# Kernel tuning notes

Hardware: AMD Instinct MI355X
Metric: run time of the kernel (lower is better)

Reference implementation:

```python
import jax, jax.numpy as jnp
import numpy as np

INPUT_DIM = 1024
NUM_HEADS = 16
HEAD_DIM = INPUT_DIM // NUM_HEADS


def setup_inputs() -> dict:
    key = jax.random.key(0)
    ks = jax.random.split(key, 9)
    d = INPUT_DIM
    s = 1.0 / np.sqrt(d)
    x = jax.random.normal(ks[0], (2, 2048, d), dtype=jnp.float32)
    # nn.Linear default init ~ U(-1/sqrt(in), 1/sqrt(in)); weights stored as (out, in), we keep (in, out)
    Wq = jax.random.uniform(ks[1], (d, d), jnp.float32, -s, s)
    bq = jax.random.uniform(ks[2], (d,), jnp.float32, -s, s)
    Wk = jax.random.uniform(ks[3], (d, d), jnp.float32, -s, s)
    bk = jax.random.uniform(ks[4], (d,), jnp.float32, -s, s)
    Wv = jax.random.uniform(ks[5], (d, d), jnp.float32, -s, s)
    bv = jax.random.uniform(ks[6], (d,), jnp.float32, -s, s)
    Wo = jax.random.uniform(ks[7], (d, d), jnp.float32, -s, s)
    bo = jax.random.uniform(ks[8], (d,), jnp.float32, -s, s)
    return {"x": x, "Wq": Wq, "bq": bq, "Wk": Wk, "bk": bk, "Wv": Wv, "bv": bv, "Wo": Wo, "bo": bo}


def reference(x, Wq, bq, Wk, bk, Wv, bv, Wo, bo):
    b, t, d = x.shape
    h, hd = NUM_HEADS, HEAD_DIM
    # projections -> [b, h, t, hd]
    q = (x @ Wq + bq).reshape(b, t, h, hd).transpose(0, 2, 1, 3)
    k = (x @ Wk + bk).reshape(b, t, h, hd).transpose(0, 2, 1, 3)
    v = (x @ Wv + bv).reshape(b, t, h, hd).transpose(0, 2, 1, 3)
    scores = jnp.einsum('bhqd,bhkd->bhqk', q, k) / jnp.sqrt(jnp.float32(hd))
    probs = jax.nn.softmax(scores, axis=-1)
    out = jnp.einsum('bhqk,bhkd->bhqd', probs, v)
    out = out.transpose(0, 2, 1, 3).reshape(b, t, d)
    return out @ Wo + bo
```

## Files before the change

kernel.cpp:

```cpp
#include <hip/hip_runtime.h>
#include <math.h>


#define BATCH 2
#define SEQ   2048
#define DIM   1024
#define NHEAD 16
#define HDIM  64
#define MROWS (BATCH * SEQ)
#define BH    (BATCH * NHEAD)
#define NKT   (SEQ / 64)

typedef __attribute__((ext_vector_type(4))) float     floatx4;
typedef __attribute__((ext_vector_type(4))) float     float4v;
typedef __attribute__((ext_vector_type(8))) _Float16  half8;
typedef __attribute__((ext_vector_type(4))) _Float16  half4;
typedef __attribute__((ext_vector_type(2))) __fp16    fp16x2;
typedef __attribute__((ext_vector_type(4))) unsigned  uint4v;

#define SOFT_C 5.77078016f
#define QSCALE 0.18033688f

#if __has_builtin(__builtin_amdgcn_exp2f)
#define EXP2F(x) __builtin_amdgcn_exp2f(x)
#else
#define EXP2F(x) exp2f(x)
#endif

__device__ __forceinline__ void gload16(const void* g, void* l) {
    __builtin_amdgcn_global_load_lds(
        (const __attribute__((address_space(1))) unsigned int*)g,
        (__attribute__((address_space(3))) unsigned int*)l, 16, 0, 0);
}

__device__ __forceinline__ unsigned pk2(float a, float b) {
    fp16x2 v = __builtin_amdgcn_cvt_pkrtz(a, b);
    return __builtin_bit_cast(unsigned, v);
}

__device__ __forceinline__ void plswap(unsigned &a, unsigned &b) {
#if __has_builtin(__builtin_amdgcn_permlane32_swap) && __has_builtin(__builtin_amdgcn_permlane16_swap)
    auto r32 = __builtin_amdgcn_permlane32_swap(a, b, false, false);
    auto r16 = __builtin_amdgcn_permlane16_swap(r32[0], r32[1], false, false);
    a = r16[0]; b = r16[1];
#else
    asm volatile("s_nop 1\n\t"
                 "v_permlane32_swap_b32 %0, %1\n\t"
                 "s_nop 1\n\t"
                 "v_permlane16_swap_b32 %0, %1\n\t"
                 "s_nop 1"
                 : "+v"(a), "+v"(b));
#endif
}

__global__ __launch_bounds__(256) void prep(
    const float* __restrict__ x,
    const float* __restrict__ Wq, const float* __restrict__ Wk,
    const float* __restrict__ Wv, const float* __restrict__ Wo,
    _Float16* __restrict__ xh,
    _Float16* __restrict__ Wqt, _Float16* __restrict__ Wkt,
    _Float16* __restrict__ Wvt, _Float16* __restrict__ Wot)
{
    const int tid = threadIdx.x;
    if (blockIdx.z == 4) {
        const int bid = blockIdx.y * 16 + blockIdx.x;
        #pragma unroll
        for (int it = 0; it < 8; ++it) {
            const size_t i = (((size_t)it * 256 + bid) * 256 + tid) * 8;
            float4v a = *(const float4v*)(x + i);
            float4v b = *(const float4v*)(x + i + 4);
            half8 o;
            #pragma unroll
            for (int c = 0; c < 4; ++c) { o[c] = (_Float16)a[c]; o[4+c] = (_Float16)b[c]; }
            *(half8*)(xh + i) = o;
        }
        return;
    }
    __shared__ float tile[64][65];
    const float* W; _Float16* o;
    switch (blockIdx.z) {
        case 0: W = Wq; o = Wqt; break;
        case 1: W = Wk; o = Wkt; break;
        case 2: W = Wv; o = Wvt; break;
        default: W = Wo; o = Wot; break;
    }
    const int n0 = blockIdx.x * 64, k0 = blockIdx.y * 64;
    #pragma unroll
    for (int p = 0; p < 16; ++p) {
        int idx = tid + p * 256;
        int r = idx >> 6, c = idx & 63;
        tile[r][c] = W[(size_t)(k0 + r) * DIM + n0 + c];
    }
    __syncthreads();
    #pragma unroll
    for (int p = 0; p < 16; ++p) {
        int idx = tid + p * 256;
        int r = idx >> 6, c = idx & 63;
        o[(size_t)(n0 + r) * DIM + k0 + c] = (_Float16)tile[c][r];
    }
}

__device__ __forceinline__ void gemm_core16(
    const _Float16* __restrict__ Ap, const _Float16* __restrict__ Bp,
    int m0, int n0, _Float16* AL, _Float16* BL, floatx4 acc[4][4])
{
    const int tid  = threadIdx.x;
    const int wave = tid >> 6;
    const int lane = tid & 63;
    const int li   = lane & 15;
    const int quad = lane >> 4;
    const int wm   = (wave >> 1) * 64;
    const int wn   = (wave & 1) * 64;

    for (int kt = 0; kt < DIM / 64; ++kt) {
        __syncthreads();
        const int k0 = kt * 64;
        #pragma unroll
        for (int p = 0; p < 4; ++p) {
            int s = tid + p * 256;
            int r = s >> 3, ks = s & 7;
            int kg = (ks ^ (r & 7)) << 3;
            int ldsb = (wave * 64 + p * 256) * 8;
            gload16(Ap + (size_t)(m0 + r) * DIM + k0 + kg, AL + ldsb);
            gload16(Bp + (size_t)(n0 + r) * DIM + k0 + kg, BL + ldsb);
        }
        __syncthreads();

        half8 a[4][2], b[4][2];
        #pragma unroll
        for (int i = 0; i < 4; ++i) {
            int ra = (wm + i * 16 + li) << 6;
            int rb = (wn + i * 16 + li) << 6;
            #pragma unroll
            for (int h = 0; h < 2; ++h) {
                a[i][h] = *(const half8*)(AL + ra + (((h * 4 + quad) ^ (li & 7)) << 3));
                b[i][h] = *(const half8*)(BL + rb + (((h * 4 + quad) ^ (li & 7)) << 3));
            }
        }
        #pragma unroll
        for (int i = 0; i < 4; ++i)
            #pragma unroll
            for (int j = 0; j < 4; ++j) {
                acc[i][j] = __builtin_amdgcn_mfma_f32_16x16x32_f16(a[i][0], b[j][0], acc[i][j], 0, 0, 0);
                acc[i][j] = __builtin_amdgcn_mfma_f32_16x16x32_f16(a[i][1], b[j][1], acc[i][j], 0, 0, 0);
            }
    }
}

__global__ __launch_bounds__(256, 2) void qkv_mfma(
    const _Float16* __restrict__ xh,
    const _Float16* __restrict__ Wqt, const _Float16* __restrict__ Wkt,
    const _Float16* __restrict__ Wvt,
    const float* __restrict__ bq, const float* __restrict__ bk,
    const float* __restrict__ bv,
    _Float16* __restrict__ Qh, _Float16* __restrict__ Kh,
    _Float16* __restrict__ Vth)
{
    __shared__ __align__(16) _Float16 SH[128 * 128];
    _Float16* AL = SH;
    _Float16* BL = SH + 128 * 64;

    const int bid = blockIdx.x + 8 * (blockIdx.y + 32 * blockIdx.z);
    const int swz = (bid & 7) * 96 + (bid >> 3);
    const int bx  = swz & 7;
    const int by  = (swz >> 3) & 31;
    const int z   = swz >> 8;

    const _Float16* Bp; const float* bias;
    if (z == 0)      { Bp = Wqt; bias = bq; }
    else if (z == 1) { Bp = Wkt; bias = bk; }
    else             { Bp = Wvt; bias = bv; }

    const int m0 = by * 128, n0 = bx * 128;

    floatx4 acc[4][4];
    #pragma unroll
    for (int i = 0; i < 4; ++i)
        #pragma unroll
        for (int j = 0; j < 4; ++j) acc[i][j] = (floatx4){0.f, 0.f, 0.f, 0.f};

    gemm_core16(xh, Bp, m0, n0, AL, BL, acc);

    const int tid = threadIdx.x, wave = tid >> 6, lane = tid & 63;
    const int li = lane & 15, quad = lane >> 4;
    const int wm = (wave >> 1) * 64, wn = (wave & 1) * 64;
    const int bb = m0 >> 11, t0 = m0 & 2047;

    if (z != 2) {
        _Float16* out = (z == 0) ? Qh : Kh;
        const float sc = (z == 0) ? QSCALE : 1.0f;
        #pragma unroll
        for (int i = 0; i < 4; ++i)
            #pragma unroll
            for (int j = 0; j < 4; ++j) {
                int n = n0 + wn + j * 16 + li;
                int h = n >> 6, hd = n & 63;
                float b_ = bias[n];
                #pragma unroll
                for (int r = 0; r < 4; ++r) {
                    int m = m0 + wm + i * 16 + quad * 4 + r;
                    int t = m & 2047;
                    out[(((size_t)(bb * NHEAD + h) * SEQ) + t) * HDIM + hd] =
                        (_Float16)((acc[i][j][r] + b_) * sc);
                }
            }
    } else {
        __syncthreads();
        #pragma unroll
        for (int i = 0; i < 4; ++i)
            #pragma unroll
            for (int j = 0; j < 4; ++j) {
                int n = wn + j * 16 + li;
                float b_ = bias[n0 + n];
                half4 w;
                #pragma unroll
                for (int r = 0; r < 4; ++r) w[r] = (_Float16)(acc[i][j][r] + b_);
                int col  = wm + i * 16 + quad * 4;
                int colp = ((((col >> 3) ^ (n & 7)) << 3)) | (col & 7);
                *(half4*)(SH + n * 128 + colp) = w;
            }
        __syncthreads();
        #pragma unroll
        for (int p = 0; p < 8; ++p) {
            int idx = p * 256 + tid;
            int v = idx >> 4, c8 = (idx & 15) * 8;
            int c8p = (((c8 >> 3) ^ (v & 7)) << 3);
            half8 w = *(const half8*)(SH + v * 128 + c8p);
            int n = n0 + v;
            int h = n >> 6, hd = n & 63;
            *(half8*)(Vth + ((size_t)(bb * NHEAD + h) * HDIM + hd) * SEQ + t0 + c8) = w;
        }
    }
}

__global__ __launch_bounds__(256, 2) void attn(
    const _Float16* __restrict__ Q, const _Float16* __restrict__ K,
    const _Float16* __restrict__ Vt,
    _Float16* __restrict__ Ctx)
{
    __shared__ __align__(16) _Float16 Ks[2][64 * 64];
    __shared__ __align__(16) _Float16 Vs[2][64 * 64];

    const int tid  = threadIdx.x;
    const int wave = tid >> 6;
    const int lane = tid & 63;
    const int li   = lane & 15;
    const int quad = lane >> 4;

    const int bid = blockIdx.x + 16 * blockIdx.y;
    const int swz = (bid & 7) * 64 + (bid >> 3);
    const int q0  = (swz & 15) * 128;
    const int bh  = swz >> 4;
    const int b   = bh >> 4, h = bh & 15;

    half8 qa[2][2];
    #pragma unroll
    for (int nq = 0; nq < 2; ++nq) {
        size_t qrow = ((size_t)bh * SEQ + q0 + wave * 32 + nq * 16 + li) * HDIM;
        qa[nq][0] = *(const half8*)(Q + qrow + quad * 8);
        qa[nq][1] = *(const half8*)(Q + qrow + 32 + quad * 8);
    }

    half8 onesA;
    {
        _Float16 v = (li == 0) ? (_Float16)1.0f : (_Float16)0.0f;
        #pragma unroll
        for (int c = 0; c < 8; ++c) onesA[c] = v;
    }

    floatx4 O[4][2];
    floatx4 rsacc[2];
    #pragma unroll
    for (int nq = 0; nq < 2; ++nq) {
        rsacc[nq] = (floatx4){0.f, 0.f, 0.f, 0.f};
        #pragma unroll
        for (int i = 0; i < 4; ++i) O[i][nq] = (floatx4){0.f, 0.f, 0.f, 0.f};
    }

    const _Float16* Kbh = K  + (size_t)bh * SEQ * HDIM;
    const _Float16* Vbh = Vt + (size_t)bh * HDIM * SEQ;

    auto stage = [&](int buf, int kt_) {
        const _Float16* Kg = Kbh + (size_t)kt_ * 64 * HDIM;
        const _Float16* Vg = Vbh + kt_ * 64;
        _Float16* Kl = &Ks[buf][0];
        _Float16* Vl = &Vs[buf][0];
        #pragma unroll
        for (int p = 0; p < 2; ++p) {
            int s = tid + p * 256;
            int r = s >> 3, ks = s & 7;
            int kg = (ks ^ (r & 7)) << 3;
            int ldsb = (wave * 64 + p * 256) * 8;
            gload16(Kg + r * HDIM + kg, Kl + ldsb);
            gload16(Vg + (size_t)r * SEQ + kg, Vl + ldsb);
        }
    };

    auto qk_phase = [&](const _Float16* Kc, const _Float16* Vc,
                        half8 (&pbN)[2][2], half8 (&vfN)[4][2]) {
        unsigned R[2][4][2];
        #pragma unroll
        for (int mb = 0; mb < 4; ++mb) {
            int row = (mb * 16 + li) << 6;
            half8 a0 = *(const half8*)(Kc + row + ((quad ^ (li & 7)) << 3));
            half8 a1 = *(const half8*)(Kc + row + (((quad + 4) ^ (li & 7)) << 3));
            #pragma unroll
            for (int nq = 0; nq < 2; ++nq) {
                floatx4 st = (floatx4){-SOFT_C, -SOFT_C, -SOFT_C, -SOFT_C};
                st = __builtin_amdgcn_mfma_f32_16x16x32_f16(a0, qa[nq][0], st, 0, 0, 0);
                st = __builtin_amdgcn_mfma_f32_16x16x32_f16(a1, qa[nq][1], st, 0, 0, 0);
                R[nq][mb][0] = pk2(EXP2F(st[0]), EXP2F(st[1]));
                R[nq][mb][1] = pk2(EXP2F(st[2]), EXP2F(st[3]));
            }
        }
        #pragma unroll
        for (int nq = 0; nq < 2; ++nq)
            #pragma unroll
            for (int f = 0; f < 2; ++f) {
                unsigned w0, w1, w2, w3;
                {
                    unsigned x = R[nq][2 * f][0], y = R[nq][2 * f + 1][0];
                    plswap(x, y);
                    w0 = x; w2 = y;
                }
                {
                    unsigned x = R[nq][2 * f][1], y = R[nq][2 * f + 1][1];
                    plswap(x, y);
                    w1 = x; w3 = y;
                }
                uint4v uw; uw[0] = w0; uw[1] = w1; uw[2] = w2; uw[3] = w3;
                pbN[nq][f] = __builtin_bit_cast(half8, uw);
            }
        #pragma unroll
        for (int mb = 0; mb < 4; ++mb) {
            int row = (mb * 16 + li) << 6;
            vfN[mb][0] = *(const half8*)(Vc + row + ((quad ^ (li & 7)) << 3));
            vfN[mb][1] = *(const half8*)(Vc + row + (((quad + 4) ^ (li & 7)) << 3));
        }
    };

    auto pv_phase = [&](half8 (&pbP)[2][2], half8 (&vfP)[4][2]) {
        #pragma unroll
        for (int nq = 0; nq < 2; ++nq) {
            rsacc[nq] = __builtin_amdgcn_mfma_f32_16x16x32_f16(onesA, pbP[nq][0], rsacc[nq], 0, 0, 0);
            rsacc[nq] = __builtin_amdgcn_mfma_f32_16x16x32_f16(onesA, pbP[nq][1], rsacc[nq], 0, 0, 0);
        }
        #pragma unroll
        for (int mb = 0; mb < 4; ++mb)
            #pragma unroll
            for (int nq = 0; nq < 2; ++nq) {
                O[mb][nq] = __builtin_amdgcn_mfma_f32_16x16x32_f16(vfP[mb][0], pbP[nq][0], O[mb][nq], 0, 0, 0);
                O[mb][nq] = __builtin_amdgcn_mfma_f32_16x16x32_f16(vfP[mb][1], pbP[nq][1], O[mb][nq], 0, 0, 0);
            }
    };

    half8 pbA[2][2], pbB[2][2];
    half8 vfA[4][2], vfB[4][2];

    stage(0, 0);
    __syncthreads();

    stage(1, 1);
    __builtin_amdgcn_s_setprio(1);
    qk_phase(&Ks[0][0], &Vs[0][0], pbA, vfA);
    __builtin_amdgcn_s_setprio(0);
    __syncthreads();

    for (int kt = 1; kt < NKT - 1; kt += 2) {
        stage(0, kt + 1);
        __builtin_amdgcn_s_setprio(1);
        pv_phase(pbA, vfA);
        qk_phase(&Ks[1][0], &Vs[1][0], pbB, vfB);
        __builtin_amdgcn_s_setprio(0);
        __syncthreads();

        stage(1, kt + 2);
        __builtin_amdgcn_s_setprio(1);
        pv_phase(pbB, vfB);
        qk_phase(&Ks[0][0], &Vs[0][0], pbA, vfA);
        __builtin_amdgcn_s_setprio(0);
        __syncthreads();
    }

    __builtin_amdgcn_s_setprio(1);
    pv_phase(pbA, vfA);
    qk_phase(&Ks[1][0], &Vs[1][0], pbB, vfB);
    pv_phase(pbB, vfB);
    __builtin_amdgcn_s_setprio(0);
    __syncthreads();

    float inv[2];
    #pragma unroll
    for (int nq = 0; nq < 2; ++nq) {
        float rs = __shfl(rsacc[nq][0], li, 64);
        inv[nq] = 1.0f / rs;
    }

    _Float16* Sw = &Ks[0][0] + wave * (32 * 64);
    #pragma unroll
    for (int mb = 0; mb < 4; ++mb)
        #pragma unroll
        for (int nq = 0; nq < 2; ++nq) {
            uint2 w;
            w.x = pk2(O[mb][nq][0] * inv[nq], O[mb][nq][1] * inv[nq]);
            w.y = pk2(O[mb][nq][2] * inv[nq], O[mb][nq][3] * inv[nq]);
            int row = nq * 16 + li;
            int col = mb * 16 + quad * 4;
            int swc = (((col >> 3) ^ (row & 7)) << 3) | (col & 7);
            *(uint2*)(Sw + row * 64 + swc) = w;
        }
    __builtin_amdgcn_s_waitcnt(0);
    #pragma unroll
    for (int p = 0; p < 4; ++p) {
        int idx = p * 64 + lane;
        int qq = idx >> 3, c = idx & 7;
        half8 v = *(const half8*)(Sw + qq * 64 + ((c ^ (qq & 7)) << 3));
        size_t row = (size_t)b * SEQ + q0 + wave * 32 + qq;
        *(half8*)(Ctx + row * DIM + h * HDIM + c * 8) = v;
    }
}

__global__ __launch_bounds__(256, 2) void out_mfma(
    const _Float16* __restrict__ Ctx, const _Float16* __restrict__ Wot,
    const float* __restrict__ bo, float* __restrict__ out)
{
    __shared__ __align__(16) _Float16 AL[128 * 64];
    __shared__ __align__(16) _Float16 BL[128 * 64];

    const int bid = blockIdx.x + 8 * blockIdx.y;
    const int swz = (bid & 7) * 32 + (bid >> 3);
    const int m0 = (swz >> 3) * 128, n0 = (swz & 7) * 128;

    floatx4 acc[4][4];
    #pragma unroll
    for (int i = 0; i < 4; ++i)
        #pragma unroll
        for (int j = 0; j < 4; ++j) acc[i][j] = (floatx4){0.f, 0.f, 0.f, 0.f};

    gemm_core16(Ctx, Wot, m0, n0, AL, BL, acc);

    const int tid = threadIdx.x, wave = tid >> 6, lane = tid & 63;
    const int li = lane & 15, quad = lane >> 4;
    const int wm = (wave >> 1) * 64, wn = (wave & 1) * 64;

    #pragma unroll
    for (int i = 0; i < 4; ++i)
        #pragma unroll
        for (int j = 0; j < 4; ++j) {
            int n = n0 + wn + j * 16 + li;
            float b_ = bo[n];
            #pragma unroll
            for (int r = 0; r < 4; ++r) {
                int m = m0 + wm + i * 16 + quad * 4 + r;
                out[(size_t)m * DIM + n] = acc[i][j][r] + b_;
            }
        }
}

extern "C" void kernel_launch(void* const* d_in, const int* in_sizes, int n_in,
                              void* d_out, int out_size, void* d_ws, size_t ws_size,
                              hipStream_t stream) {
    const float* x  = (const float*)d_in[0];
    const float* Wq = (const float*)d_in[1];
    const float* bq = (const float*)d_in[2];
    const float* Wk = (const float*)d_in[3];
    const float* bk = (const float*)d_in[4];
    const float* Wv = (const float*)d_in[5];
    const float* bv = (const float*)d_in[6];
    const float* Wo = (const float*)d_in[7];
    const float* bo = (const float*)d_in[8];
    float* out = (float*)d_out;

    const size_t PX = (size_t)MROWS * DIM;
    const size_t PW = (size_t)DIM * DIM;
    _Float16* xh  = (_Float16*)d_ws;
    _Float16* Wqt = xh + PX;
    _Float16* Wkt = Wqt + PW;
    _Float16* Wvt = Wkt + PW;
    _Float16* Wot = Wvt + PW;
    _Float16* Qh  = Wot + PW;
    _Float16* Kh  = Qh + PX;
    _Float16* spare = Kh + PX;
    _Float16* Vth = spare + PX;

    _Float16* Ctx = xh;

    prep<<<dim3(16, 16, 5), 256, 0, stream>>>(
        x, Wq, Wk, Wv, Wo, xh, Wqt, Wkt, Wvt, Wot);

    qkv_mfma<<<dim3(DIM / 128, MROWS / 128, 3), 256, 0, stream>>>(
        xh, Wqt, Wkt, Wvt, bq, bk, bv, Qh, Kh, Vth);

    attn<<<dim3(SEQ / 128, BH), 256, 0, stream>>>(
        Qh, Kh, Vth, Ctx);

    out_mfma<<<dim3(DIM / 128, MROWS / 128), 256, 0, stream>>>(
        Ctx, Wot, bo, out);
}
```

Baseline: 177.7 us.

## Double-buffer GEMM LDS tiles with K=32 steps and overlap loads with MFMA

Replaces the single-buffered K=64 GEMM mainloop in the QKV and output projection kernels with a double-buffered K=32 pipeline. The next tile's global-to-LDS load is issued before computing the current tile, and s_setprio raises wave priority around the MFMA block. The goal is to hide global load latency that previously sat behind two barriers per K step. In exchange it takes more barriers per K element, uses smaller MFMA batches per sync, and needs a new swizzle for 32-wide rows.

```diff
diff --git a/kernel.cpp b/kernel.cpp
--- a/kernel.cpp
+++ b/kernel.cpp
@@ -100,9 +100,9 @@
     }
 }
 
-__device__ __forceinline__ void gemm_core16(
+__device__ __forceinline__ void gemm_core32(
     const _Float16* __restrict__ Ap, const _Float16* __restrict__ Bp,
-    int m0, int n0, _Float16* AL, _Float16* BL, floatx4 acc[4][4])
+    int m0, int n0, _Float16* SH, floatx4 acc[4][4])
 {
     const int tid  = threadIdx.x;
     const int wave = tid >> 6;
@@ -112,38 +112,52 @@
     const int wm   = (wave >> 1) * 64;
     const int wn   = (wave & 1) * 64;
 
-    for (int kt = 0; kt < DIM / 64; ++kt) {
-        __syncthreads();
-        const int k0 = kt * 64;
-        #pragma unroll
-        for (int p = 0; p < 4; ++p) {
+    _Float16* AL0 = SH;
+    _Float16* BL0 = SH + 4096;
+    _Float16* AL1 = SH + 8192;
+    _Float16* BL1 = SH + 12288;
+
+    auto stg = [&](int k0, _Float16* AL, _Float16* BL) {
+        #pragma unroll
+        for (int p = 0; p < 2; ++p) {
             int s = tid + p * 256;
-            int r = s >> 3, ks = s & 7;
-            int kg = (ks ^ (r & 7)) << 3;
+            int r = s >> 2, ks = s & 3;
+            int kg = (ks ^ ((r >> 1) & 3)) << 3;
             int ldsb = (wave * 64 + p * 256) * 8;
             gload16(Ap + (size_t)(m0 + r) * DIM + k0 + kg, AL + ldsb);
             gload16(Bp + (size_t)(n0 + r) * DIM + k0 + kg, BL + ldsb);
         }
+    };
+
+    auto cmp = [&](const _Float16* AL, const _Float16* BL) {
+        half8 a[4], b[4];
+        const int cs = (quad ^ ((li >> 1) & 3)) << 3;
+        #pragma unroll
+        for (int i = 0; i < 4; ++i) {
+            a[i] = *(const half8*)(AL + ((wm + i * 16 + li) << 5) + cs);
+            b[i] = *(const half8*)(BL + ((wn + i * 16 + li) << 5) + cs);
+        }
+        #pragma unroll
+        for (int i = 0; i < 4; ++i)
+            #pragma unroll
+            for (int j = 0; j < 4; ++j)
+                acc[i][j] = __builtin_amdgcn_mfma_f32_16x16x32_f16(a[i], b[j], acc[i][j], 0, 0, 0);
+    };
+
+    stg(0, AL0, BL0);
+    __syncthreads();
+
+    for (int kt = 0; kt < DIM / 32; kt += 2) {
+        stg((kt + 1) * 32, AL1, BL1);
+        __builtin_amdgcn_s_setprio(1);
+        cmp(AL0, BL0);
+        __builtin_amdgcn_s_setprio(0);
         __syncthreads();
-
-        half8 a[4][2], b[4][2];
-        #pragma unroll
-        for (int i = 0; i < 4; ++i) {
-            int ra = (wm + i * 16 + li) << 6;
-            int rb = (wn + i * 16 + li) << 6;
-            #pragma unroll
-            for (int h = 0; h < 2; ++h) {
-                a[i][h] = *(const half8*)(AL + ra + (((h * 4 + quad) ^ (li & 7)) << 3));
-                b[i][h] = *(const half8*)(BL + rb + (((h * 4 + quad) ^ (li & 7)) << 3));
-            }
-        }
-        #pragma unroll
-        for (int i = 0; i < 4; ++i)
-            #pragma unroll
-            for (int j = 0; j < 4; ++j) {
-                acc[i][j] = __builtin_amdgcn_mfma_f32_16x16x32_f16(a[i][0], b[j][0], acc[i][j], 0, 0, 0);
-                acc[i][j] = __builtin_amdgcn_mfma_f32_16x16x32_f16(a[i][1], b[j][1], acc[i][j], 0, 0, 0);
-            }
+        if (kt + 2 < DIM / 32) stg((kt + 2) * 32, AL0, BL0);
+        __builtin_amdgcn_s_setprio(1);
+        cmp(AL1, BL1);
+        __builtin_amdgcn_s_setprio(0);
+        __syncthreads();
     }
 }
 
@@ -157,8 +171,6 @@
     _Float16* __restrict__ Vth)
 {
     __shared__ __align__(16) _Float16 SH[128 * 128];
-    _Float16* AL = SH;
-    _Float16* BL = SH + 128 * 64;
 
     const int bid = blockIdx.x + 8 * (blockIdx.y + 32 * blockIdx.z);
     const int swz = (bid & 7) * 96 + (bid >> 3);
@@ -179,7 +191,7 @@
         #pragma unroll
         for (int j = 0; j < 4; ++j) acc[i][j] = (floatx4){0.f, 0.f, 0.f, 0.f};
 
-    gemm_core16(xh, Bp, m0, n0, AL, BL, acc);
+    gemm_core32(xh, Bp, m0, n0, SH, acc);
 
     const int tid = threadIdx.x, wave = tid >> 6, lane = tid & 63;
     const int li = lane & 15, quad = lane >> 4;
@@ -424,8 +436,7 @@
     const _Float16* __restrict__ Ctx, const _Float16* __restrict__ Wot,
     const float* __restrict__ bo, float* __restrict__ out)
 {
-    __shared__ __align__(16) _Float16 AL[128 * 64];
-    __shared__ __align__(16) _Float16 BL[128 * 64];
+    __shared__ __align__(16) _Float16 SH[4 * 4096];
 
     const int bid = blockIdx.x + 8 * blockIdx.y;
     const int swz = (bid & 7) * 32 + (bid >> 3);
@@ -437,7 +448,7 @@
         #pragma unroll
         for (int j = 0; j < 4; ++j) acc[i][j] = (floatx4){0.f, 0.f, 0.f, 0.f};
 
-    gemm_core16(Ctx, Wot, m0, n0, AL, BL, acc);
+    gemm_core32(Ctx, Wot, m0, n0, SH, acc);
 
     const int tid = threadIdx.x, wave = tid >> 6, lane = tid & 63;
     const int li = lane & 15, quad = lane >> 4;
```

Result: no change. 178.1 us (+0.3%).
